# Performance work log

Measured on AMD Instinct MI355X. Metric: run time of the kernel, lower is better.

The kernel has to match this reference:

```python
import jax, jax.numpy as jnp
from jax import lax
import numpy as np

B, NROI, WS, CH = 2, 1024, 5, 18
E = WS * WS            # embed_dim = 25
HID = E * CH           # hidden_dim = 450


def setup_inputs() -> dict:
    key = jax.random.key(0)
    ks = jax.random.split(key, 16)
    f32 = jnp.float32
    rn = lambda k, shape, s=0.05: jax.random.normal(k, shape, f32) * s
    inp = {}
    inp['feat_fv_raw'] = jax.random.normal(ks[0], (B, 128, 64, 512), f32)
    inp['feat_bev_raw'] = jax.random.normal(ks[1], (B, 512, 200, 176), f32)
    # rois: (x0, y0, z0, dx, dy, dz, theta) in KITTI-like ranges
    u = jax.random.uniform(ks[2], (B, NROI, 7), f32)
    inp['rois'] = jnp.stack([
        u[..., 0] * 70.4,            # x0 in [0, 70.4]
        u[..., 1] * 80.0 - 40.0,     # y0 in [-40, 40]
        u[..., 2] * 2.5 - 2.0,       # z0 in [-2, 0.5]
        1.0 + 3.0 * u[..., 3],       # dx
        1.0 + 3.0 * u[..., 4],       # dy
        0.5 + 1.5 * u[..., 5],       # dz
        u[..., 6] * np.pi], axis=-1) # theta
    # pre_roi_pros_fv / bev (conv3x3 -> BN(eval) -> ReLU -> conv1x1)
    inp['fv_w1'] = rn(ks[3], (18, 128, 3, 3)); inp['fv_b1'] = jnp.zeros(18, f32)
    inp['fv_gamma'] = jnp.ones(18, f32); inp['fv_beta'] = jnp.zeros(18, f32)
    inp['fv_mean'] = jnp.zeros(18, f32); inp['fv_var'] = jnp.ones(18, f32)
    inp['fv_w2'] = rn(ks[4], (18, 18, 1, 1)); inp['fv_b2'] = jnp.zeros(18, f32)
    inp['bev_w1'] = rn(ks[5], (18, 512, 3, 3)); inp['bev_b1'] = jnp.zeros(18, f32)
    inp['bev_gamma'] = jnp.ones(18, f32); inp['bev_beta'] = jnp.zeros(18, f32)
    inp['bev_mean'] = jnp.zeros(18, f32); inp['bev_var'] = jnp.ones(18, f32)
    inp['bev_w2'] = rn(ks[6], (18, 18, 1, 1)); inp['bev_b2'] = jnp.zeros(18, f32)
    # shared MultiHeadSelfAttention (embed_dim=25, num_heads=5)
    inp['Wq'] = rn(ks[7], (E, E), 0.2); inp['bq'] = jnp.zeros(E, f32)
    inp['Wk'] = rn(ks[8], (E, E), 0.2); inp['bk'] = jnp.zeros(E, f32)
    inp['Wv'] = rn(ks[9], (E, E), 0.2); inp['bv'] = jnp.zeros(E, f32)
    inp['Wf'] = rn(ks[10], (E, E), 0.2); inp['bf'] = jnp.zeros(E, f32)
    # classifier head: Conv2d(36,18,3,p=1), fc1(450->225), fc2(225->3)
    inp['conv_w'] = rn(ks[11], (18, 36, 3, 3)); inp['conv_b'] = jnp.zeros(18, f32)
    inp['fc1_w'] = rn(ks[12], (HID // 2, HID)); inp['fc1_b'] = jnp.zeros(HID // 2, f32)
    inp['fc2_w'] = rn(ks[13], (3, HID // 2)); inp['fc2_b'] = jnp.zeros(3, f32)
    return inp


def _conv2d(x, w, b):
    p = (w.shape[2] - 1) // 2
    out = lax.conv_general_dilated(x, w, (1, 1), [(p, p), (p, p)],
                                   dimension_numbers=('NCHW', 'OIHW', 'NCHW'))
    return out + b[None, :, None, None]


def _pre(x, w1, b1, g, be, mu, var, w2, b2):
    x = _conv2d(x, w1, b1)
    x = (x - mu[None, :, None, None]) * (g / jnp.sqrt(var + 1e-3))[None, :, None, None] + be[None, :, None, None]
    return _conv2d(jax.nn.relu(x), w2, b2)


def _gen_box(roi):
    x0, y0, z0, x, y, z, th = [roi[:, i] for i in range(7)]
    c, s = jnp.cos(th), jnp.sin(th)
    x1 = x0 - (y * c + x * s) / 2; x2 = x0 + (y * c + x * s) / 2
    y1 = y0 - (y * s + x * c) / 2; y2 = y0 + (y * s + x * c) / 2
    z1 = z0 - z / 2; z2 = z0 + z / 2
    return jnp.stack([z1, x1, z2, x2], 1), jnp.stack([y1, x1, y2, x2], 1)


def _grids(bbox, is_bev):
    t = jnp.linspace(0.0, 1.0, WS)
    gz = bbox[:, 0:1] + t[None, :] * (bbox[:, 2:3] - bbox[:, 0:1])  # [N,5]
    gx = bbox[:, 1:2] + t[None, :] * (bbox[:, 3:4] - bbox[:, 1:2])
    gz = gz / 40.0 if is_bev else (gz + 1.0) / 2.0
    gx = (gx - 35.2) / 35.2
    n = bbox.shape[0]
    GZ = jnp.broadcast_to(gz[:, :, None], (n, WS, WS))  # meshgrid 'ij'
    GX = jnp.broadcast_to(gx[:, None, :], (n, WS, WS))
    return jnp.stack([GZ, GX], -1)  # [...,0]=x(width) coord, [...,1]=y(height) coord


def _grid_sample_nearest(feat, grids):
    # feat [C,H,W]; grids [N,5,5,2]; matches torch grid_sample(nearest, align_corners=True, zeros)
    C, H, W = feat.shape
    ix = jnp.round((grids[..., 0] + 1.0) * 0.5 * (W - 1))
    iy = jnp.round((grids[..., 1] + 1.0) * 0.5 * (H - 1))
    valid = (ix >= 0) & (ix <= W - 1) & (iy >= 0) & (iy <= H - 1)
    ixc = jnp.clip(ix, 0, W - 1).astype(jnp.int32)
    iyc = jnp.clip(iy, 0, H - 1).astype(jnp.int32)
    out = feat[:, iyc, ixc]                       # [C,N,5,5]
    out = jnp.where(valid[None], out, 0.0)
    return jnp.transpose(out, (1, 0, 2, 3))       # [N,C,5,5]


def _mhsa(feat1, feat2, Wq, bq, Wk, bk, Wv, bv, Wf, bf, nh=WS):
    N, T, Ed = feat1.shape
    hd = Ed // nh
    heads = lambda x, W, b: (x @ W.T + b).reshape(N, T, nh, hd).transpose(0, 2, 1, 3)
    q, k, v = heads(feat2, Wq, bq), heads(feat1, Wk, bk), heads(feat2, Wv, bv)
    attn = jax.nn.softmax(jnp.einsum('nhqd,nhkd->nhqk', q, k) / jnp.sqrt(jnp.float32(hd)), axis=-1)
    av = jnp.einsum('nhqk,nhkd->nhqd', attn, v).transpose(0, 2, 1, 3).reshape(N, T, Ed)
    return av @ Wf.T + bf + feat1


def _classifier(bev, fv, Wq, bq, Wk, bk, Wv, bv, Wf, bf, conv_w, conv_b, fc1_w, fc1_b, fc2_w, fc2_b):
    N = bev.shape[0]
    x1 = _mhsa(bev, fv, Wq, bq, Wk, bk, Wv, bv, Wf, bf).reshape(N, CH, WS, WS)
    x2 = _mhsa(fv, bev, Wq, bq, Wk, bk, Wv, bv, Wf, bf).reshape(N, CH, WS, WS)
    x = jnp.concatenate([x1, x2], axis=1)
    x = _conv2d(x, conv_w, conv_b).reshape(N, HID)
    x = jax.nn.relu(x @ fc1_w.T + fc1_b)
    return x @ fc2_w.T + fc2_b


def _logits(feat_fv_raw, feat_bev_raw, rois, fv_w1, fv_b1, fv_gamma, fv_beta, fv_mean, fv_var, fv_w2, fv_b2,
            bev_w1, bev_b1, bev_gamma, bev_beta, bev_mean, bev_var, bev_w2, bev_b2,
            Wq, bq, Wk, bk, Wv, bv, Wf, bf, conv_w, conv_b, fc1_w, fc1_b, fc2_w, fc2_b):
    ffv = _pre(feat_fv_raw, fv_w1, fv_b1, fv_gamma, fv_beta, fv_mean, fv_var, fv_w2, fv_b2)
    fbev = _pre(feat_bev_raw, bev_w1, bev_b1, bev_gamma, bev_beta, bev_mean, bev_var, bev_w2, bev_b2)

    def per_sample(ffv1, fbev1, roi):
        bfv, bbev = _gen_box(roi)
        sfv = _grid_sample_nearest(ffv1, _grids(bfv, False)).reshape(-1, CH, E)
        sbev = _grid_sample_nearest(fbev1, _grids(bbev, True)).reshape(-1, CH, E)
        return _classifier(sbev, sfv, Wq, bq, Wk, bk, Wv, bv, Wf, bf,
                           conv_w, conv_b, fc1_w, fc1_b, fc2_w, fc2_b)

    return jax.vmap(per_sample)(ffv, fbev, rois)  # [B, NROI, 3]


def reference(feat_fv_raw, feat_bev_raw, rois, fv_w1, fv_b1, fv_gamma, fv_beta, fv_mean, fv_var, fv_w2, fv_b2,
              bev_w1, bev_b1, bev_gamma, bev_beta, bev_mean, bev_var, bev_w2, bev_b2,
              Wq, bq, Wk, bk, Wv, bv, Wf, bf, conv_w, conv_b, fc1_w, fc1_b, fc2_w, fc2_b):
    logits = _logits(feat_fv_raw, feat_bev_raw, rois, fv_w1, fv_b1, fv_gamma, fv_beta, fv_mean, fv_var,
                     fv_w2, fv_b2, bev_w1, bev_b1, bev_gamma, bev_beta, bev_mean, bev_var, bev_w2, bev_b2,
                     Wq, bq, Wk, bk, Wv, bv, Wf, bf, conv_w, conv_b, fc1_w, fc1_b, fc2_w, fc2_b)
    preds = jnp.argmax(logits, axis=-1) + 1          # cls_pred per batch sample
    scores = jax.nn.softmax(logits, axis=-1)          # box_scores per batch sample
    return preds, scores
```

## Files before the change

kernel.cpp:

```cpp
#include <hip/hip_runtime.h>
#include <math.h>

__global__ void transpose_w_kernel(const float* __restrict__ w, float* __restrict__ wt, int C) {
  int idx = blockIdx.x * blockDim.x + threadIdx.x;
  int total = 18 * C * 9;
  if (idx >= total) return;
  int co = idx / (C * 9);
  int rem = idx % (C * 9);
  int ci = rem / 9;
  int tap = rem % 9;
  wt[(ci * 9 + tap) * 18 + co] = w[idx];
}

__global__ void transpose_fc1_kernel(const float* __restrict__ w, float* __restrict__ wt) {
  int idx = blockIdx.x * blockDim.x + threadIdx.x;
  if (idx >= 225 * 450) return;
  int o = idx / 450;
  int i = idx % 450;
  wt[i * 256 + o] = w[idx];
}

__global__ __launch_bounds__(256) void pre_merged_kernel(
    const float* __restrict__ xF, const float* __restrict__ wtF,
    const float* __restrict__ b1F, const float* __restrict__ gF,
    const float* __restrict__ beF, const float* __restrict__ muF,
    const float* __restrict__ vF, const float* __restrict__ w2F,
    const float* __restrict__ b2F, float* __restrict__ outF,
    const float* __restrict__ xB, const float* __restrict__ wtB,
    const float* __restrict__ b1B, const float* __restrict__ gB,
    const float* __restrict__ beB, const float* __restrict__ muB,
    const float* __restrict__ vB, const float* __restrict__ w2B,
    const float* __restrict__ b2B, float* __restrict__ outB) {
  int flat = blockIdx.x;
  const float *x, *wt, *b1, *gamma, *beta, *mean, *var, *w2, *b2;
  float* out;
  int H, W, cs, xt, h, b;
  if (flat < 1200) {
    xt = flat % 3; h = (flat / 3) % 200; b = flat / 600;
    x = xB; wt = wtB; b1 = b1B; gamma = gB; beta = beB; mean = muB; var = vB;
    w2 = w2B; b2 = b2B; out = outB;
    H = 200; W = 176; cs = 128;
  } else {
    int f = flat - 1200;
    xt = f & 7; h = (f >> 3) & 63; b = f >> 9;
    x = xF; wt = wtF; b1 = b1F; gamma = gF; beta = beF; mean = muF; var = vF;
    w2 = w2F; b2 = b2F; out = outF;
    H = 64; W = 512; cs = 32;
  }

  int tid = threadIdx.x;
  int pixel = tid & 63;
  int split = __builtin_amdgcn_readfirstlane(tid >> 6);
  int w = xt * 64 + pixel;
  bool active = (w < W);

  float acc[18];
#pragma unroll
  for (int i = 0; i < 18; i++) acc[i] = 0.f;

  const float* xb = x + (size_t)b * (cs * 4) * H * W;
  int ci0 = split * cs;
  for (int ci = 0; ci < cs; ci++) {
    const float* plane = xb + (size_t)(ci0 + ci) * H * W;
#pragma unroll
    for (int dh = 0; dh < 3; dh++) {
      int r = h + dh - 1;
      if ((unsigned)r < (unsigned)H) {
        const float* row = plane + (size_t)r * W;
        float v0 = (active && w >= 1) ? row[w - 1] : 0.f;
        float v1 = active ? row[w] : 0.f;
        float v2 = (active && w + 1 < W) ? row[w + 1] : 0.f;
        const float* wp = wt + ((size_t)(ci0 + ci) * 9 + dh * 3) * 18;
#pragma unroll
        for (int co = 0; co < 18; co++) acc[co] = fmaf(v0, wp[co], acc[co]);
#pragma unroll
        for (int co = 0; co < 18; co++) acc[co] = fmaf(v1, wp[18 + co], acc[co]);
#pragma unroll
        for (int co = 0; co < 18; co++) acc[co] = fmaf(v2, wp[36 + co], acc[co]);
      }
    }
  }

  __shared__ float red[3][64][19];
  if (split > 0) {
#pragma unroll
    for (int co = 0; co < 18; co++) red[split - 1][pixel][co] = acc[co];
  }
  __syncthreads();
  if (split == 0 && active) {
#pragma unroll
    for (int s = 0; s < 3; s++)
#pragma unroll
      for (int co = 0; co < 18; co++) acc[co] += red[s][pixel][co];
    float y[18];
#pragma unroll
    for (int co = 0; co < 18; co++) {
      float sc = gamma[co] / sqrtf(var[co] + 1e-3f);
      y[co] = fmaxf((acc[co] + b1[co] - mean[co]) * sc + beta[co], 0.f);
    }
    size_t obase = (size_t)b * 18 * H * W + (size_t)h * W + w;
#pragma unroll
    for (int co2 = 0; co2 < 18; co2++) {
      float s2 = b2[co2];
#pragma unroll
      for (int c = 0; c < 18; c++) s2 = fmaf(y[c], w2[co2 * 18 + c], s2);
      out[obase + (size_t)co2 * H * W] = s2;
    }
  }
}

__global__ __launch_bounds__(256) void classifier_kernel(
    const float* __restrict__ ffv, const float* __restrict__ fbev,
    const float* __restrict__ rois, const float* __restrict__ Wq,
    const float* __restrict__ bq, const float* __restrict__ Wk,
    const float* __restrict__ bk, const float* __restrict__ Wv,
    const float* __restrict__ bv, const float* __restrict__ Wf,
    const float* __restrict__ bf, const float* __restrict__ conv_w,
    const float* __restrict__ conv_b, const float* __restrict__ wt_fc1,
    const float* __restrict__ fc1_b, const float* __restrict__ fc2_w,
    const float* __restrict__ fc2_b, float* __restrict__ out) {
  int rid = blockIdx.x;
  int b = rid >> 10;
  int tid = threadIdx.x;

  __shared__ __align__(16) float sW[4 * 25 * 28];
  __shared__ float sB[100];
  __shared__ __align__(16) float sfv[18 * 28], sbev[18 * 28];
  __shared__ __align__(16) float pr[6 * 18 * 28];
  __shared__ __align__(16) float av[2 * 18 * 28];
  __shared__ __align__(16) float xx[2 * 18 * 28];
  __shared__ __align__(16) float hid[452];
  __shared__ float h1r[226];
  __shared__ float lg[3];
  __shared__ int c_ixf[25], c_iyf[25], c_vf[25];
  __shared__ int c_ixb[25], c_iyb[25], c_vb[25];

  for (int t = tid; t < 625; t += 256) {
    int j = t / 25, i = t % 25;
    sW[(0 * 25 + j) * 28 + i] = Wq[t];
    sW[(1 * 25 + j) * 28 + i] = Wk[t];
    sW[(2 * 25 + j) * 28 + i] = Wv[t];
    sW[(3 * 25 + j) * 28 + i] = Wf[t];
  }
  if (tid < 25) {
    sB[tid] = bq[tid];
    sB[25 + tid] = bk[tid];
    sB[50 + tid] = bv[tid];
    sB[75 + tid] = bf[tid];
  }

  if (tid < 25) {
    const float* roi = rois + (size_t)rid * 7;
    double x0 = roi[0], y0 = roi[1], z0 = roi[2];
    double dx = roi[3], dy = roi[4], dz = roi[5], th = roi[6];
    double c = cos(th), s = sin(th);
    double half1 = (dy * c + dx * s) / 2.0;
    double half2 = (dy * s + dx * c) / 2.0;
    double bx1 = x0 - half1, bx2 = x0 + half1;
    double by1 = y0 - half2, by2 = y0 + half2;
    double bz1 = z0 - dz / 2.0, bz2 = z0 + dz / 2.0;
    int i = tid / 5, j = tid % 5;
    double ti = i * 0.25, tj = j * 0.25;
    double gz = bz1 + ti * (bz2 - bz1);
    gz = (gz + 1.0) / 2.0;
    double gx = bx1 + tj * (bx2 - bx1);
    gx = (gx - 35.2) / 35.2;
    double ixf = rint((gz + 1.0) * 0.5 * 511.0);
    double iyf = rint((gx + 1.0) * 0.5 * 63.0);
    c_vf[tid] = (ixf >= 0.0) && (ixf <= 511.0) && (iyf >= 0.0) && (iyf <= 63.0);
    c_ixf[tid] = (int)fmin(fmax(ixf, 0.0), 511.0);
    c_iyf[tid] = (int)fmin(fmax(iyf, 0.0), 63.0);
    double gzb = (by1 + ti * (by2 - by1)) / 40.0;
    double ixb = rint((gzb + 1.0) * 0.5 * 175.0);
    double iyb = rint((gx + 1.0) * 0.5 * 199.0);
    c_vb[tid] = (ixb >= 0.0) && (ixb <= 175.0) && (iyb >= 0.0) && (iyb <= 199.0);
    c_ixb[tid] = (int)fmin(fmax(ixb, 0.0), 175.0);
    c_iyb[tid] = (int)fmin(fmax(iyb, 0.0), 199.0);
  }
  __syncthreads();

  {
    const float* fvb = ffv + (size_t)b * 18 * 64 * 512;
    const float* bvb = fbev + (size_t)b * 18 * 200 * 176;
    for (int item = tid; item < 900; item += 256) {
      if (item < 450) {
        int ch = item / 25, pos = item % 25;
        sfv[ch * 28 + pos] = c_vf[pos] ? fvb[((size_t)ch * 64 + c_iyf[pos]) * 512 + c_ixf[pos]] : 0.f;
      } else {
        int it = item - 450;
        int ch = it / 25, pos = it % 25;
        sbev[ch * 28 + pos] = c_vb[pos] ? bvb[((size_t)ch * 200 + c_iyb[pos]) * 176 + c_ixb[pos]] : 0.f;
      }
    }
  }
  __syncthreads();

  for (int idx = tid; idx < 450; idx += 256) {
    int t = idx / 25, j = idx % 25;
    const float4* xa4 = (const float4*)(sfv + t * 28);
    const float4* xb4 = (const float4*)(sbev + t * 28);
    const float4* wq4 = (const float4*)(sW + (0 * 25 + j) * 28);
    const float4* wk4 = (const float4*)(sW + (1 * 25 + j) * 28);
    const float4* wv4 = (const float4*)(sW + (2 * 25 + j) * 28);
    float aqf = sB[j], akf = sB[25 + j], avf = sB[50 + j];
    float aqb = sB[j], akb = sB[25 + j], avb = sB[50 + j];
#pragma unroll
    for (int k = 0; k < 6; k++) {
      float4 xa = xa4[k], xb = xb4[k];
      float4 wq = wq4[k], wk = wk4[k], wv = wv4[k];
      aqf = fmaf(xa.w, wq.w, fmaf(xa.z, wq.z, fmaf(xa.y, wq.y, fmaf(xa.x, wq.x, aqf))));
      akf = fmaf(xa.w, wk.w, fmaf(xa.z, wk.z, fmaf(xa.y, wk.y, fmaf(xa.x, wk.x, akf))));
      avf = fmaf(xa.w, wv.w, fmaf(xa.z, wv.z, fmaf(xa.y, wv.y, fmaf(xa.x, wv.x, avf))));
      aqb = fmaf(xb.w, wq.w, fmaf(xb.z, wq.z, fmaf(xb.y, wq.y, fmaf(xb.x, wq.x, aqb))));
      akb = fmaf(xb.w, wk.w, fmaf(xb.z, wk.z, fmaf(xb.y, wk.y, fmaf(xb.x, wk.x, akb))));
      avb = fmaf(xb.w, wv.w, fmaf(xb.z, wv.z, fmaf(xb.y, wv.y, fmaf(xb.x, wv.x, avb))));
    }
    {
      float xa = sfv[t * 28 + 24], xb = sbev[t * 28 + 24];
      float wq = sW[(0 * 25 + j) * 28 + 24], wk = sW[(1 * 25 + j) * 28 + 24],
            wv = sW[(2 * 25 + j) * 28 + 24];
      aqf = fmaf(xa, wq, aqf); akf = fmaf(xa, wk, akf); avf = fmaf(xa, wv, avf);
      aqb = fmaf(xb, wq, aqb); akb = fmaf(xb, wk, akb); avb = fmaf(xb, wv, avb);
    }
    pr[(0 * 18 + t) * 28 + j] = aqf;
    pr[(1 * 18 + t) * 28 + j] = akf;
    pr[(2 * 18 + t) * 28 + j] = avf;
    pr[(3 * 18 + t) * 28 + j] = aqb;
    pr[(4 * 18 + t) * 28 + j] = akb;
    pr[(5 * 18 + t) * 28 + j] = avb;
  }
  __syncthreads();

  const float rs5 = 0.44721359549995793f;
  if (tid < 90) {
    int hh = tid / 18, t = tid % 18;
#pragma unroll
    for (int m = 0; m < 2; m++) {
      const float* q = pr + (m == 0 ? 0 : 3) * 18 * 28;
      const float* k = pr + (m == 0 ? 4 : 1) * 18 * 28;
      const float* v = pr + (m == 0 ? 2 : 5) * 18 * 28;
      float p_[18];
      float mx = -1e30f;
#pragma unroll
      for (int ss = 0; ss < 18; ss++) {
        float sc = 0.f;
#pragma unroll
        for (int d = 0; d < 5; d++)
          sc = fmaf(q[t * 28 + hh * 5 + d], k[ss * 28 + hh * 5 + d], sc);
        sc *= rs5;
        p_[ss] = sc;
        mx = fmaxf(mx, sc);
      }
      float sm = 0.f;
#pragma unroll
      for (int ss = 0; ss < 18; ss++) {
        p_[ss] = expf(p_[ss] - mx);
        sm += p_[ss];
      }
      float inv = 1.f / sm;
#pragma unroll
      for (int d = 0; d < 5; d++) {
        float a = 0.f;
#pragma unroll
        for (int ss = 0; ss < 18; ss++)
          a = fmaf(p_[ss], v[ss * 28 + hh * 5 + d], a);
        av[(m * 18 + t) * 28 + hh * 5 + d] = a * inv;
      }
    }
  }
  __syncthreads();

  for (int idx = tid; idx < 450; idx += 256) {
    int t = idx / 25, j = idx % 25;
    const float4* wf4 = (const float4*)(sW + (3 * 25 + j) * 28);
    const float4* a04 = (const float4*)(av + (0 * 18 + t) * 28);
    const float4* a14 = (const float4*)(av + (1 * 18 + t) * 28);
    float s1 = sB[75 + j] + sbev[t * 28 + j];
    float s2 = sB[75 + j] + sfv[t * 28 + j];
#pragma unroll
    for (int k = 0; k < 6; k++) {
      float4 wf = wf4[k], a0 = a04[k], a1 = a14[k];
      s1 = fmaf(a0.w, wf.w, fmaf(a0.z, wf.z, fmaf(a0.y, wf.y, fmaf(a0.x, wf.x, s1))));
      s2 = fmaf(a1.w, wf.w, fmaf(a1.z, wf.z, fmaf(a1.y, wf.y, fmaf(a1.x, wf.x, s2))));
    }
    {
      float wf = sW[(3 * 25 + j) * 28 + 24];
      s1 = fmaf(av[(0 * 18 + t) * 28 + 24], wf, s1);
      s2 = fmaf(av[(1 * 18 + t) * 28 + 24], wf, s2);
    }
    xx[(0 * 18 + t) * 28 + j] = s1;
    xx[(1 * 18 + t) * 28 + j] = s2;
  }
  __syncthreads();

  for (int idx = tid; idx < 450; idx += 256) {
    int co = idx / 25, pos = idx % 25, pi = pos / 5, pj = pos % 5;
    float acc = conv_b[co];
    for (int ci = 0; ci < 36; ci++) {
      const float* xc = (ci < 18) ? &xx[ci * 28] : &xx[(18 + ci - 18 + 18) * 28 - 18 * 28 + (ci - 18) * 28 + 18 * 28 - (ci - 18) * 28];
      xc = (ci < 18) ? &xx[(0 * 18 + ci) * 28] : &xx[(1 * 18 + (ci - 18)) * 28];
      const float* wp = conv_w + ((size_t)co * 36 + ci) * 9;
#pragma unroll
      for (int dh = 0; dh < 3; dh++) {
        int rr = pi + dh - 1;
        if ((unsigned)rr < 5u) {
#pragma unroll
          for (int dw = 0; dw < 3; dw++) {
            int cc = pj + dw - 1;
            if ((unsigned)cc < 5u) acc = fmaf(xc[rr * 5 + cc], wp[dh * 3 + dw], acc);
          }
        }
      }
    }
    hid[idx] = acc;
  }
  __syncthreads();

  if (tid < 225) {
    int o = tid;
    float a0 = fc1_b[o], a1 = 0.f, a2 = 0.f, a3 = 0.f;
    const float4* h4 = (const float4*)hid;
    for (int k = 0; k < 112; k++) {
      float4 hv = h4[k];
      int i = k * 4;
      a0 = fmaf(hv.x, wt_fc1[(size_t)i * 256 + o], a0);
      a1 = fmaf(hv.y, wt_fc1[(size_t)(i + 1) * 256 + o], a1);
      a2 = fmaf(hv.z, wt_fc1[(size_t)(i + 2) * 256 + o], a2);
      a3 = fmaf(hv.w, wt_fc1[(size_t)(i + 3) * 256 + o], a3);
    }
    a0 = fmaf(hid[448], wt_fc1[(size_t)448 * 256 + o], a0);
    a1 = fmaf(hid[449], wt_fc1[(size_t)449 * 256 + o], a1);
    h1r[o] = fmaxf((a0 + a1) + (a2 + a3), 0.f);
  }
  __syncthreads();

  int wave = tid >> 6, lane = tid & 63;
  if (wave < 3) {
    const float* wr = fc2_w + (size_t)wave * 225;
    float p = 0.f;
#pragma unroll
    for (int k = 0; k < 4; k++) {
      int i = lane + k * 64;
      if (i < 225) p = fmaf(h1r[i], wr[i], p);
    }
#pragma unroll
    for (int m = 32; m >= 1; m >>= 1) p += __shfl_xor(p, m);
    if (lane == 0) lg[wave] = p + fc2_b[wave];
  }
  __syncthreads();

  if (tid == 0) {
    float l0 = lg[0], l1 = lg[1], l2 = lg[2];
    int arg = 0;
    float bm = l0;
    if (l1 > bm) { arg = 1; bm = l1; }
    if (l2 > bm) { arg = 2; bm = l2; }
    float m = fmaxf(l0, fmaxf(l1, l2));
    float e0 = expf(l0 - m), e1 = expf(l1 - m), e2 = expf(l2 - m);
    float inv = 1.f / (e0 + e1 + e2);
    out[rid] = (float)(arg + 1);
    float* sc = out + 2048 + (size_t)rid * 3;
    sc[0] = e0 * inv;
    sc[1] = e1 * inv;
    sc[2] = e2 * inv;
  }
}

extern "C" void kernel_launch(void* const* d_in, const int* in_sizes, int n_in,
                              void* d_out, int out_size, void* d_ws, size_t ws_size,
                              hipStream_t stream) {
  const float* feat_fv = (const float*)d_in[0];
  const float* feat_bev = (const float*)d_in[1];
  const float* rois = (const float*)d_in[2];
  const float* fv_w1 = (const float*)d_in[3];
  const float* fv_b1 = (const float*)d_in[4];
  const float* fv_gamma = (const float*)d_in[5];
  const float* fv_beta = (const float*)d_in[6];
  const float* fv_mean = (const float*)d_in[7];
  const float* fv_var = (const float*)d_in[8];
  const float* fv_w2 = (const float*)d_in[9];
  const float* fv_b2 = (const float*)d_in[10];
  const float* bev_w1 = (const float*)d_in[11];
  const float* bev_b1 = (const float*)d_in[12];
  const float* bev_gamma = (const float*)d_in[13];
  const float* bev_beta = (const float*)d_in[14];
  const float* bev_mean = (const float*)d_in[15];
  const float* bev_var = (const float*)d_in[16];
  const float* bev_w2 = (const float*)d_in[17];
  const float* bev_b2 = (const float*)d_in[18];
  const float* Wq = (const float*)d_in[19];
  const float* bq = (const float*)d_in[20];
  const float* Wk = (const float*)d_in[21];
  const float* bk = (const float*)d_in[22];
  const float* Wv = (const float*)d_in[23];
  const float* bv = (const float*)d_in[24];
  const float* Wf = (const float*)d_in[25];
  const float* bf = (const float*)d_in[26];
  const float* conv_w = (const float*)d_in[27];
  const float* conv_b = (const float*)d_in[28];
  const float* fc1_w = (const float*)d_in[29];
  const float* fc1_b = (const float*)d_in[30];
  const float* fc2_w = (const float*)d_in[31];
  const float* fc2_b = (const float*)d_in[32];

  float* ws = (float*)d_ws;
  float* ffv = ws;
  float* fbev = ffv + 1179648;
  float* wt_fv = fbev + 1267200;
  float* wt_bev = wt_fv + 20736;
  float* wt_fc1 = wt_bev + 82944;

  transpose_w_kernel<<<(18 * 128 * 9 + 255) / 256, 256, 0, stream>>>(fv_w1, wt_fv, 128);
  transpose_w_kernel<<<(18 * 512 * 9 + 255) / 256, 256, 0, stream>>>(bev_w1, wt_bev, 512);
  transpose_fc1_kernel<<<(225 * 450 + 255) / 256, 256, 0, stream>>>(fc1_w, wt_fc1);

  pre_merged_kernel<<<2224, 256, 0, stream>>>(
      feat_fv, wt_fv, fv_b1, fv_gamma, fv_beta, fv_mean, fv_var, fv_w2, fv_b2, ffv,
      feat_bev, wt_bev, bev_b1, bev_gamma, bev_beta, bev_mean, bev_var, bev_w2, bev_b2, fbev);

  classifier_kernel<<<2048, 256, 0, stream>>>(
      ffv, fbev, rois, Wq, bq, Wk, bk, Wv, bv, Wf, bf, conv_w, conv_b, wt_fc1,
      fc1_b, fc2_w, fc2_b, (float*)d_out);
}
```

Measured before the change: 394.5 us.

## Split BEV conv channels into equal chunks with partial-sum reduce kernel

Splits the 512-channel BEV 3x3 conv into four 128-channel chunks so every work item processes 32 channels per wave, matching the FV work. The items are distributed round-robin over 2048 persistent-style blocks, removing the load imbalance where BEV blocks did four times the work of FV blocks. BEV partial sums are written to a workspace and a new reduce kernel sums them and applies BN, ReLU and the 1x1 conv. This adds an extra launch and partial-buffer traffic, and it relies on the workspace being large enough for the partial buffer.

```diff
diff --git a/kernel.cpp b/kernel.cpp
--- a/kernel.cpp
+++ b/kernel.cpp
@@ -20,92 +20,134 @@
   wt[i * 256 + o] = w[idx];
 }
 
-__global__ __launch_bounds__(256) void pre_merged_kernel(
+__global__ __launch_bounds__(256) void pre_chunk_kernel(
     const float* __restrict__ xF, const float* __restrict__ wtF,
     const float* __restrict__ b1F, const float* __restrict__ gF,
     const float* __restrict__ beF, const float* __restrict__ muF,
     const float* __restrict__ vF, const float* __restrict__ w2F,
     const float* __restrict__ b2F, float* __restrict__ outF,
     const float* __restrict__ xB, const float* __restrict__ wtB,
-    const float* __restrict__ b1B, const float* __restrict__ gB,
-    const float* __restrict__ beB, const float* __restrict__ muB,
-    const float* __restrict__ vB, const float* __restrict__ w2B,
-    const float* __restrict__ b2B, float* __restrict__ outB) {
-  int flat = blockIdx.x;
-  const float *x, *wt, *b1, *gamma, *beta, *mean, *var, *w2, *b2;
-  float* out;
-  int H, W, cs, xt, h, b;
-  if (flat < 1200) {
-    xt = flat % 3; h = (flat / 3) % 200; b = flat / 600;
-    x = xB; wt = wtB; b1 = b1B; gamma = gB; beta = beB; mean = muB; var = vB;
-    w2 = w2B; b2 = b2B; out = outB;
-    H = 200; W = 176; cs = 128;
-  } else {
-    int f = flat - 1200;
-    xt = f & 7; h = (f >> 3) & 63; b = f >> 9;
-    x = xF; wt = wtF; b1 = b1F; gamma = gF; beta = beF; mean = muF; var = vF;
-    w2 = w2F; b2 = b2F; out = outF;
-    H = 64; W = 512; cs = 32;
-  }
-
+    float* __restrict__ partial) {
   int tid = threadIdx.x;
   int pixel = tid & 63;
   int split = __builtin_amdgcn_readfirstlane(tid >> 6);
+
+  __shared__ float red[3][64][19];
+
+  for (int k = 0; k < 3; ++k) {
+    int li = (blockIdx.x >> 3) + k * 256;
+    if (li >= 728) break;
+    int c = (blockIdx.x & 7) * 728 + li;
+
+    const float *x, *wt;
+    int H, W, xt, h, b, cig, C;
+    bool isBev;
+    if (c < 4800) {
+      int rest = c >> 2;
+      cig = c & 3;
+      xt = rest % 3; h = (rest / 3) % 200; b = rest / 600;
+      x = xB; wt = wtB; H = 200; W = 176; C = 512; isBev = true;
+    } else {
+      int f = c - 4800;
+      cig = 0;
+      xt = f & 7; h = (f >> 3) & 63; b = f >> 9;
+      x = xF; wt = wtF; H = 64; W = 512; C = 128; isBev = false;
+    }
+
+    int w = xt * 64 + pixel;
+    bool active = (w < W);
+
+    float acc[18];
+#pragma unroll
+    for (int i = 0; i < 18; i++) acc[i] = 0.f;
+
+    const float* xb = x + (size_t)b * C * H * W;
+    int ci0 = cig * 128 + split * 32;
+    for (int ci = 0; ci < 32; ci++) {
+      const float* plane = xb + (size_t)(ci0 + ci) * H * W;
+#pragma unroll
+      for (int dh = 0; dh < 3; dh++) {
+        int r = h + dh - 1;
+        if ((unsigned)r < (unsigned)H) {
+          const float* row = plane + (size_t)r * W;
+          float v0 = (active && w >= 1) ? row[w - 1] : 0.f;
+          float v1 = active ? row[w] : 0.f;
+          float v2 = (active && w + 1 < W) ? row[w + 1] : 0.f;
+          const float* wp = wt + ((size_t)(ci0 + ci) * 9 + dh * 3) * 18;
+#pragma unroll
+          for (int co = 0; co < 18; co++) acc[co] = fmaf(v0, wp[co], acc[co]);
+#pragma unroll
+          for (int co = 0; co < 18; co++) acc[co] = fmaf(v1, wp[18 + co], acc[co]);
+#pragma unroll
+          for (int co = 0; co < 18; co++) acc[co] = fmaf(v2, wp[36 + co], acc[co]);
+        }
+      }
+    }
+
+    __syncthreads();
+    if (split > 0) {
+#pragma unroll
+      for (int co = 0; co < 18; co++) red[split - 1][pixel][co] = acc[co];
+    }
+    __syncthreads();
+    if (split == 0) {
+#pragma unroll
+      for (int s = 0; s < 3; s++)
+#pragma unroll
+        for (int co = 0; co < 18; co++) acc[co] += red[s][pixel][co];
+      if (isBev) {
+        float* pb = partial + (size_t)c * 1152;
+#pragma unroll
+        for (int co = 0; co < 18; co++) pb[co * 64 + pixel] = acc[co];
+      } else if (active) {
+        float y[18];
+#pragma unroll
+        for (int co = 0; co < 18; co++) {
+          float sc = gF[co] / sqrtf(vF[co] + 1e-3f);
+          y[co] = fmaxf((acc[co] + b1F[co] - muF[co]) * sc + beF[co], 0.f);
+        }
+        size_t obase = (size_t)b * 18 * H * W + (size_t)h * W + w;
+#pragma unroll
+        for (int co2 = 0; co2 < 18; co2++) {
+          float s2 = b2F[co2];
+#pragma unroll
+          for (int cc = 0; cc < 18; cc++) s2 = fmaf(y[cc], w2F[co2 * 18 + cc], s2);
+          outF[obase + (size_t)co2 * H * W] = s2;
+        }
+      }
+    }
+  }
+}
+
+__global__ __launch_bounds__(256) void bev_reduce_kernel(
+    const float* __restrict__ partial, const float* __restrict__ b1,
+    const float* __restrict__ gamma, const float* __restrict__ beta,
+    const float* __restrict__ mean, const float* __restrict__ var,
+    const float* __restrict__ w2, const float* __restrict__ b2,
+    float* __restrict__ out) {
+  int idx = blockIdx.x * 256 + threadIdx.x;
+  if (idx >= 76800) return;
+  int pixel = idx & 63;
+  int rest = idx >> 6;
+  int xt = rest % 3, h = (rest / 3) % 200, b = rest / 600;
   int w = xt * 64 + pixel;
-  bool active = (w < W);
-
-  float acc[18];
-#pragma unroll
-  for (int i = 0; i < 18; i++) acc[i] = 0.f;
-
-  const float* xb = x + (size_t)b * (cs * 4) * H * W;
-  int ci0 = split * cs;
-  for (int ci = 0; ci < cs; ci++) {
-    const float* plane = xb + (size_t)(ci0 + ci) * H * W;
-#pragma unroll
-    for (int dh = 0; dh < 3; dh++) {
-      int r = h + dh - 1;
-      if ((unsigned)r < (unsigned)H) {
-        const float* row = plane + (size_t)r * W;
-        float v0 = (active && w >= 1) ? row[w - 1] : 0.f;
-        float v1 = active ? row[w] : 0.f;
-        float v2 = (active && w + 1 < W) ? row[w + 1] : 0.f;
-        const float* wp = wt + ((size_t)(ci0 + ci) * 9 + dh * 3) * 18;
-#pragma unroll
-        for (int co = 0; co < 18; co++) acc[co] = fmaf(v0, wp[co], acc[co]);
-#pragma unroll
-        for (int co = 0; co < 18; co++) acc[co] = fmaf(v1, wp[18 + co], acc[co]);
-#pragma unroll
-        for (int co = 0; co < 18; co++) acc[co] = fmaf(v2, wp[36 + co], acc[co]);
-      }
-    }
-  }
-
-  __shared__ float red[3][64][19];
-  if (split > 0) {
-#pragma unroll
-    for (int co = 0; co < 18; co++) red[split - 1][pixel][co] = acc[co];
-  }
-  __syncthreads();
-  if (split == 0 && active) {
-#pragma unroll
-    for (int s = 0; s < 3; s++)
-#pragma unroll
-      for (int co = 0; co < 18; co++) acc[co] += red[s][pixel][co];
-    float y[18];
-#pragma unroll
-    for (int co = 0; co < 18; co++) {
-      float sc = gamma[co] / sqrtf(var[co] + 1e-3f);
-      y[co] = fmaxf((acc[co] + b1[co] - mean[co]) * sc + beta[co], 0.f);
-    }
-    size_t obase = (size_t)b * 18 * H * W + (size_t)h * W + w;
-#pragma unroll
-    for (int co2 = 0; co2 < 18; co2++) {
-      float s2 = b2[co2];
-#pragma unroll
-      for (int c = 0; c < 18; c++) s2 = fmaf(y[c], w2[co2 * 18 + c], s2);
-      out[obase + (size_t)co2 * H * W] = s2;
-    }
+  if (w >= 176) return;
+  const float* p0 = partial + (size_t)rest * 4 * 1152;
+  float y[18];
+#pragma unroll
+  for (int co = 0; co < 18; co++) {
+    int o = co * 64 + pixel;
+    float a = p0[o] + p0[1152 + o] + p0[2304 + o] + p0[3456 + o];
+    float sc = gamma[co] / sqrtf(var[co] + 1e-3f);
+    y[co] = fmaxf((a + b1[co] - mean[co]) * sc + beta[co], 0.f);
+  }
+  size_t obase = (size_t)b * 18 * 200 * 176 + (size_t)h * 176 + w;
+#pragma unroll
+  for (int co2 = 0; co2 < 18; co2++) {
+    float s2 = b2[co2];
+#pragma unroll
+    for (int c = 0; c < 18; c++) s2 = fmaf(y[c], w2[co2 * 18 + c], s2);
+    out[obase + (size_t)co2 * 200 * 176] = s2;
   }
 }
 
@@ -297,8 +339,7 @@
     int co = idx / 25, pos = idx % 25, pi = pos / 5, pj = pos % 5;
     float acc = conv_b[co];
     for (int ci = 0; ci < 36; ci++) {
-      const float* xc = (ci < 18) ? &xx[ci * 28] : &xx[(18 + ci - 18 + 18) * 28 - 18 * 28 + (ci - 18) * 28 + 18 * 28 - (ci - 18) * 28];
-      xc = (ci < 18) ? &xx[(0 * 18 + ci) * 28] : &xx[(1 * 18 + (ci - 18)) * 28];
+      const float* xc = (ci < 18) ? &xx[(0 * 18 + ci) * 28] : &xx[(1 * 18 + (ci - 18)) * 28];
       const float* wp = conv_w + ((size_t)co * 36 + ci) * 9;
 #pragma unroll
       for (int dh = 0; dh < 3; dh++) {
@@ -409,14 +450,18 @@
   float* wt_fv = fbev + 1267200;
   float* wt_bev = wt_fv + 20736;
   float* wt_fc1 = wt_bev + 82944;
+  float* partial = wt_fc1 + 115200;
 
   transpose_w_kernel<<<(18 * 128 * 9 + 255) / 256, 256, 0, stream>>>(fv_w1, wt_fv, 128);
   transpose_w_kernel<<<(18 * 512 * 9 + 255) / 256, 256, 0, stream>>>(bev_w1, wt_bev, 512);
   transpose_fc1_kernel<<<(225 * 450 + 255) / 256, 256, 0, stream>>>(fc1_w, wt_fc1);
 
-  pre_merged_kernel<<<2224, 256, 0, stream>>>(
+  pre_chunk_kernel<<<2048, 256, 0, stream>>>(
       feat_fv, wt_fv, fv_b1, fv_gamma, fv_beta, fv_mean, fv_var, fv_w2, fv_b2, ffv,
-      feat_bev, wt_bev, bev_b1, bev_gamma, bev_beta, bev_mean, bev_var, bev_w2, bev_b2, fbev);
+      feat_bev, wt_bev, partial);
+
+  bev_reduce_kernel<<<300, 256, 0, stream>>>(
+      partial, bev_b1, bev_gamma, bev_beta, bev_mean, bev_var, bev_w2, bev_b2, fbev);
 
   classifier_kernel<<<2048, 256, 0, stream>>>(
       ffv, fbev, rois, Wq, bq, Wk, bk, Wv, bv, Wf, bf, conv_w, conv_b, wt_fc1,
```

New measurement: 436.9 us. 10.8% more time.
